# Kernel tuning notes

Hardware: AMD Instinct MI355X
Metric: run time of the kernel (lower is better)

The kernel has to match this reference:

```python
import jax, jax.numpy as jnp
import numpy as np

BATCH = 8192
IN_FEATURES = 1024
OUT_FEATURES = 1024
GRID_SIZE = 5
SPLINE_ORDER = 3
GRID_MIN, GRID_MAX = -1.0, 1.0
NUM_BASES = GRID_SIZE + SPLINE_ORDER  # 8
GRID_LEN = GRID_SIZE + 2 * SPLINE_ORDER + 1  # 12


def setup_inputs() -> dict:
    key = jax.random.key(0)
    k1, k2, k3 = jax.random.split(key, 3)
    x = jax.random.normal(k1, (BATCH, IN_FEATURES), dtype=jnp.float32)
    base_weight = jax.random.normal(k2, (OUT_FEATURES, IN_FEATURES), dtype=jnp.float32) * 0.1
    spline_weight = jax.random.normal(k3, (OUT_FEATURES, IN_FEATURES, NUM_BASES), dtype=jnp.float32) * 0.1
    grid = jnp.linspace(GRID_MIN, GRID_MAX, GRID_LEN, dtype=jnp.float32)  # buffer, not learned
    return {"x": x, "base_weight": base_weight, "spline_weight": spline_weight, "grid": grid}


def _bspline_basis(xc, grid, order):
    """Iterative Cox-de Boor DP, vectorized over all features and basis indices.
    xc: [B, F] clamped inputs; grid: [G] uniform knots (all denominators > 0).
    Returns [B, F, G - order - 1] = [B, F, NUM_BASES]."""
    G = grid.shape[0]
    xe = xc[..., None]  # [B, F, 1]
    # k = 0: indicator of knot interval, matches (x >= grid[i]) & (x < grid[i+1])
    B = ((xe >= grid[:-1]) & (xe < grid[1:])).astype(xc.dtype)  # [B, F, G-1]
    for k in range(1, order + 1):
        left = (xe - grid[: G - k - 1]) / (grid[k : G - 1] - grid[: G - k - 1]) * B[..., :-1]
        right = (grid[k + 1 : G] - xe) / (grid[k + 1 : G] - grid[1 : G - k]) * B[..., 1:]
        B = left + right  # [B, F, G-1-k]
    return B


def reference(x, base_weight, spline_weight, grid):
    # base path: SiLU activation then linear
    base_output = jax.nn.silu(x) @ base_weight.T  # [B, out]
    # spline path: B-spline basis per feature, weighted sum over (in, basis)
    x_clamped = jnp.clip(x, GRID_MIN * 0.99, GRID_MAX * 0.99)
    basis = _bspline_basis(x_clamped, grid, SPLINE_ORDER)  # [B, in, NUM_BASES]
    spline_output = jnp.einsum("bin,oin->bo", basis, spline_weight)
    return base_output + spline_output
```

## Files before the change

kernel.cpp:

```cpp
#include <hip/hip_runtime.h>
#include <stdint.h>

typedef _Float16 f16;
typedef __attribute__((ext_vector_type(8))) _Float16 f16x8;
typedef __attribute__((ext_vector_type(4))) float f32x4;

#define BATCH 8192
#define INF   1024
#define OUTF  1024
#define KTOT  9216
#define NT    72
#define CONV_BLOCKS 4608

__device__ __forceinline__ void gload16(const void* g, void* l) {
  __builtin_amdgcn_global_load_lds(
      (const __attribute__((address_space(1))) uint32_t*)g,
      (__attribute__((address_space(3))) uint32_t*)l, 16, 0, 0);
}

__global__ __launch_bounds__(256) void fused_prep_kernel(
    const float* __restrict__ bw, const float* __restrict__ sw,
    const float* __restrict__ x, const float* __restrict__ grid,
    f16* __restrict__ Wb, f16* __restrict__ Abuf)
{
  int blk = blockIdx.x;
  if (blk < CONV_BLOCKS) {
    int idx = blk * 256 + threadIdx.x;
    int o = idx / 1152;
    int r = idx - o * 1152;
    int k8 = r * 8;
    const float* src = (k8 < INF) ? (bw + (size_t)o * INF + k8)
                                  : (sw + (size_t)o * (INF * 8) + (k8 - INF));
    float4 v0 = *(const float4*)src;
    float4 v1 = *(const float4*)(src + 4);
    f16x8 ov;
    ov[0] = (f16)v0.x; ov[1] = (f16)v0.y; ov[2] = (f16)v0.z; ov[3] = (f16)v0.w;
    ov[4] = (f16)v1.x; ov[5] = (f16)v1.y; ov[6] = (f16)v1.z; ov[7] = (f16)v1.w;
    *(f16x8*)(Wb + (size_t)o * KTOT + k8) = ov;
    return;
  }

  int q = (blk - CONV_BLOCKS) * 256 + threadIdx.x;
  int b = q >> 8;
  int i0 = (q & 255) << 2;
  float4 xv = *(const float4*)(x + ((size_t)b << 10) + i0);
  float xa[4] = {xv.x, xv.y, xv.z, xv.w};

  float g[12];
#pragma unroll
  for (int j = 0; j < 12; ++j) g[j] = grid[j];
  float H  = g[1] - g[0];
  float r1 = 1.0f / H;
  float r2 = 0.5f * r1;
  float r3 = (1.0f / 3.0f) * r1;

  f16 sil[4];
  f16x8 bas[4];
#pragma unroll
  for (int e = 0; e < 4; ++e) {
    float v = xa[e];
    sil[e] = (f16)(v / (1.0f + __expf(-v)));
    float xe = fminf(fmaxf(v, -0.99f), 0.99f);
    float Bv[11];
#pragma unroll
    for (int j = 0; j < 11; ++j) Bv[j] = (xe >= g[j] && xe < g[j + 1]) ? 1.0f : 0.0f;
#pragma unroll
    for (int j = 0; j < 10; ++j) Bv[j] = (xe - g[j]) * r1 * Bv[j] + (g[j + 2] - xe) * r1 * Bv[j + 1];
#pragma unroll
    for (int j = 0; j < 9; ++j)  Bv[j] = (xe - g[j]) * r2 * Bv[j] + (g[j + 3] - xe) * r2 * Bv[j + 1];
#pragma unroll
    for (int j = 0; j < 8; ++j)  Bv[j] = (xe - g[j]) * r3 * Bv[j] + (g[j + 4] - xe) * r3 * Bv[j + 1];
#pragma unroll
    for (int n = 0; n < 8; ++n) bas[e][n] = (f16)Bv[n];
  }
  f16* row = Abuf + (size_t)b * KTOT;
  *(uint64_t*)(row + i0) = *(const uint64_t*)sil;
  f16* bp = row + INF + (size_t)i0 * 8;
#pragma unroll
  for (int e = 0; e < 4; ++e) *(f16x8*)(bp + e * 8) = bas[e];
}

#define LDA(base, m, s) (*(const f16x8*)((base) + (((m)*16 + la) * 64 + ((((s)*4 + lb) ^ lasw) * 8))))
#define LDB(base, n, s) (*(const f16x8*)((base) + ((wcn*64 + (n)*16 + la) * 64 + ((((s)*4 + lb) ^ lasw) * 8))))

#define MFMA1(m, n, s) acc[m][n] = __builtin_amdgcn_mfma_f32_16x16x32_f16(af[m][s], bf[n][s], acc[m][n], 0, 0, 0)
#define MFMA_S0(m0) do { \
  MFMA1(m0,0,0);   MFMA1(m0,1,0);   MFMA1(m0,2,0);   MFMA1(m0,3,0); \
  MFMA1(m0+1,0,0); MFMA1(m0+1,1,0); MFMA1(m0+1,2,0); MFMA1(m0+1,3,0); } while (0)
#define MFMA_S1(m0) do { \
  MFMA1(m0,0,1);   MFMA1(m0,1,1);   MFMA1(m0,2,1);   MFMA1(m0,3,1); \
  MFMA1(m0+1,0,1); MFMA1(m0+1,1,1); MFMA1(m0+1,2,1); MFMA1(m0+1,3,1); } while (0)

#define SCHED0 __builtin_amdgcn_sched_barrier(0)
#define SBARF  do { SCHED0; __builtin_amdgcn_s_barrier(); SCHED0; } while (0)
#define LGKM0  do { asm volatile("s_waitcnt lgkmcnt(0)" ::: "memory"); SCHED0; } while (0)

template <bool ATOMIC>
__global__ __launch_bounds__(256, 2) void kan_gemm_kernel(
    const f16* __restrict__ A, const f16* __restrict__ W,
    float* __restrict__ C, float* __restrict__ P1)
{
  __shared__ __align__(16) f16 lsA[128 * 64];
  __shared__ __align__(16) f16 lsB[256 * 64];

  const size_t K = KTOT;
  int bid = blockIdx.x;
  int xcd = bid & 7;
  int u   = bid >> 3;
  int tm  = xcd * 8 + (u & 7);
  int tn  = (u >> 3) & 3;
  int split = u >> 5;
  size_t kbase = (size_t)split * (NT * 64);

  int tid = threadIdx.x;
  int w = tid >> 6, l = tid & 63;
  int wcn = w;
  int la = l & 15, lb = l >> 4, lasw = la & 7;

  int rh = tid >> 3;
  int sc = (tid & 7) ^ (rh & 7);
  const f16* aSrc0 = A + (size_t)(tm * 128 + rh) * K + kbase + sc * 8;
  const f16* bSrc0 = W + (size_t)(tn * 256 + rh) * K + kbase + sc * 8;

  auto stageA = [&](int t) {
    size_t koff = (size_t)t * 64;
#pragma unroll
    for (int ln = 0; ln < 4; ++ln)
      gload16(aSrc0 + (size_t)ln * 32 * K + koff, lsA + ln * 2048 + w * 512);
  };
  auto stageB = [&](int t) {
    size_t koff = (size_t)t * 64;
#pragma unroll
    for (int ln = 0; ln < 8; ++ln)
      gload16(bSrc0 + (size_t)ln * 32 * K + koff, lsB + ln * 2048 + w * 512);
  };

  f16x8 af[8][2], bf[4][2];
  f32x4 acc[8][4] = {};

  stageA(0); stageB(0);

  for (int t = 0; t < NT; ++t) {
    asm volatile("s_waitcnt vmcnt(0)" ::: "memory");
    SBARF;

    bf[0][0] = LDB(lsB, 0, 0); bf[1][0] = LDB(lsB, 1, 0);
    bf[2][0] = LDB(lsB, 2, 0); bf[3][0] = LDB(lsB, 3, 0);
    bf[0][1] = LDB(lsB, 0, 1); bf[1][1] = LDB(lsB, 1, 1);
    bf[2][1] = LDB(lsB, 2, 1); bf[3][1] = LDB(lsB, 3, 1);
    af[0][0] = LDA(lsA, 0, 0); af[0][1] = LDA(lsA, 0, 1);
    af[1][0] = LDA(lsA, 1, 0); af[1][1] = LDA(lsA, 1, 1);
    __builtin_amdgcn_s_setprio(1);
    af[2][0] = LDA(lsA, 2, 0); af[3][0] = LDA(lsA, 3, 0);
    MFMA_S0(0);
    af[2][1] = LDA(lsA, 2, 1); af[3][1] = LDA(lsA, 3, 1);
    MFMA_S1(0);
    af[4][0] = LDA(lsA, 4, 0); af[5][0] = LDA(lsA, 5, 0);
    af[4][1] = LDA(lsA, 4, 1); af[5][1] = LDA(lsA, 5, 1);
    MFMA_S0(2);
    af[6][0] = LDA(lsA, 6, 0); af[7][0] = LDA(lsA, 7, 0);
    af[6][1] = LDA(lsA, 6, 1); af[7][1] = LDA(lsA, 7, 1);
    MFMA_S1(2);
    __builtin_amdgcn_s_setprio(0);

    LGKM0;
    SBARF;

    if (t < NT - 1) { stageA(t + 1); stageB(t + 1); }
    __builtin_amdgcn_s_setprio(1);
    MFMA_S0(4); MFMA_S1(4);
    MFMA_S0(6); MFMA_S1(6);
    __builtin_amdgcn_s_setprio(0);
  }

  int rowBase = tm * 128 + lb * 4;
  int colBase = tn * 256 + wcn * 64 + la;
  float* dst = ATOMIC ? C : (split ? P1 : C);
#pragma unroll
  for (int m = 0; m < 8; ++m)
#pragma unroll
    for (int n = 0; n < 4; ++n) {
      int col = colBase + n * 16;
#pragma unroll
      for (int j = 0; j < 4; ++j) {
        int row = rowBase + m * 16 + j;
        if (ATOMIC) atomicAdd(&C[(size_t)row * OUTF + col], acc[m][n][j]);
        else        dst[(size_t)row * OUTF + col] = acc[m][n][j];
      }
    }
}

__global__ __launch_bounds__(256) void reduce_kernel(
    float* __restrict__ out, const float* __restrict__ p)
{
  size_t i = ((size_t)blockIdx.x * 256 + threadIdx.x) * 4;
  f32x4 a = *(f32x4*)(out + i);
  f32x4 b = *(const f32x4*)(p + i);
  a += b;
  *(f32x4*)(out + i) = a;
}

extern "C" void kernel_launch(void* const* d_in, const int* in_sizes, int n_in,
                              void* d_out, int out_size, void* d_ws, size_t ws_size,
                              hipStream_t stream)
{
  const float* x  = (const float*)d_in[0];
  const float* bw = (const float*)d_in[1];
  const float* sw = (const float*)d_in[2];
  const float* gr = (const float*)d_in[3];
  float* out = (float*)d_out;

  f16* Wb = (f16*)d_ws;
  size_t wBytes = (size_t)OUTF * KTOT * sizeof(f16);
  f16* Abuf = (f16*)((char*)d_ws + wBytes);
  size_t aBytes = (size_t)BATCH * KTOT * sizeof(f16);
  size_t oBytes = (size_t)BATCH * OUTF * sizeof(float);

  int prepBlocks = (BATCH * INF / 4) / 256;
  fused_prep_kernel<<<CONV_BLOCKS + prepBlocks, 256, 0, stream>>>(
      bw, sw, x, gr, Wb, Abuf);

  if (ws_size >= wBytes + aBytes + oBytes) {
    float* P1 = (float*)((char*)d_ws + wBytes + aBytes);
    kan_gemm_kernel<false><<<512, 256, 0, stream>>>(Abuf, Wb, out, P1);
    reduce_kernel<<<(int)(oBytes / sizeof(float) / 4 / 256), 256, 0, stream>>>(out, P1);
  } else {
    hipMemsetAsync(d_out, 0, oBytes, stream);
    kan_gemm_kernel<true><<<512, 256, 0, stream>>>(Abuf, Wb, out, nullptr);
  }
}
```

Before: 205.6 us.

## Pre-swizzle weights into MFMA fragment layout and load B directly to registers

```diff
diff --git a/kernel.cpp b/kernel.cpp
--- a/kernel.cpp
+++ b/kernel.cpp
@@ -10,6 +10,7 @@
 #define OUTF  1024
 #define KTOT  9216
 #define NT    72
+#define NKT   144
 #define CONV_BLOCKS 4608
 
 __device__ __forceinline__ void gload16(const void* g, void* l) {
@@ -21,7 +22,7 @@
 __global__ __launch_bounds__(256) void fused_prep_kernel(
     const float* __restrict__ bw, const float* __restrict__ sw,
     const float* __restrict__ x, const float* __restrict__ grid,
-    f16* __restrict__ Wb, f16* __restrict__ Abuf)
+    f16* __restrict__ Wc, f16* __restrict__ Abuf)
 {
   int blk = blockIdx.x;
   if (blk < CONV_BLOCKS) {
@@ -36,7 +37,12 @@
     f16x8 ov;
     ov[0] = (f16)v0.x; ov[1] = (f16)v0.y; ov[2] = (f16)v0.z; ov[3] = (f16)v0.w;
     ov[4] = (f16)v1.x; ov[5] = (f16)v1.y; ov[6] = (f16)v1.z; ov[7] = (f16)v1.w;
-    *(f16x8*)(Wb + (size_t)o * KTOT + k8) = ov;
+    int tn = o >> 8, rp = o & 255;
+    int wcn = rp >> 6, n = (rp >> 4) & 3, la = rp & 15;
+    int kt = r >> 3, c = r & 7, s = c >> 2, lb = c & 3;
+    size_t off = (size_t)(tn * NKT + kt) * 16384 + wcn * 4096
+               + (s * 4 + n) * 512 + (lb * 16 + la) * 8;
+    *(f16x8*)(Wc + off) = ov;
     return;
   }
 
@@ -81,27 +87,58 @@
 }
 
 #define LDA(base, m, s) (*(const f16x8*)((base) + (((m)*16 + la) * 64 + ((((s)*4 + lb) ^ lasw) * 8))))
-#define LDB(base, n, s) (*(const f16x8*)((base) + ((wcn*64 + (n)*16 + la) * 64 + ((((s)*4 + lb) ^ lasw) * 8))))
-
-#define MFMA1(m, n, s) acc[m][n] = __builtin_amdgcn_mfma_f32_16x16x32_f16(af[m][s], bf[n][s], acc[m][n], 0, 0, 0)
-#define MFMA_S0(m0) do { \
-  MFMA1(m0,0,0);   MFMA1(m0,1,0);   MFMA1(m0,2,0);   MFMA1(m0,3,0); \
-  MFMA1(m0+1,0,0); MFMA1(m0+1,1,0); MFMA1(m0+1,2,0); MFMA1(m0+1,3,0); } while (0)
-#define MFMA_S1(m0) do { \
-  MFMA1(m0,0,1);   MFMA1(m0,1,1);   MFMA1(m0,2,1);   MFMA1(m0,3,1); \
-  MFMA1(m0+1,0,1); MFMA1(m0+1,1,1); MFMA1(m0+1,2,1); MFMA1(m0+1,3,1); } while (0)
+
+#define MFMA1(m, n, s, BF) acc[m][n] = __builtin_amdgcn_mfma_f32_16x16x32_f16(af[m][s], BF[(s)*4+(n)], acc[m][n], 0, 0, 0)
+#define MFMA_S0(m0, BF) do { \
+  MFMA1(m0,0,0,BF);   MFMA1(m0,1,0,BF);   MFMA1(m0,2,0,BF);   MFMA1(m0,3,0,BF); \
+  MFMA1(m0+1,0,0,BF); MFMA1(m0+1,1,0,BF); MFMA1(m0+1,2,0,BF); MFMA1(m0+1,3,0,BF); } while (0)
+#define MFMA_S1(m0, BF) do { \
+  MFMA1(m0,0,1,BF);   MFMA1(m0,1,1,BF);   MFMA1(m0,2,1,BF);   MFMA1(m0,3,1,BF); \
+  MFMA1(m0+1,0,1,BF); MFMA1(m0+1,1,1,BF); MFMA1(m0+1,2,1,BF); MFMA1(m0+1,3,1,BF); } while (0)
 
 #define SCHED0 __builtin_amdgcn_sched_barrier(0)
 #define SBARF  do { SCHED0; __builtin_amdgcn_s_barrier(); SCHED0; } while (0)
 #define LGKM0  do { asm volatile("s_waitcnt lgkmcnt(0)" ::: "memory"); SCHED0; } while (0)
 
+#define TILE_BODY(bfC, bfN, t) do { \
+  asm volatile("s_waitcnt vmcnt(0)" ::: "memory"); \
+  SBARF; \
+  if ((t) < NT - 1) { \
+    const f16* bp_ = bSrc + (size_t)(ktbase + (t) + 1) * 16384; \
+    bfN[0] = *(const f16x8*)(bp_);          bfN[1] = *(const f16x8*)(bp_ + 512); \
+    bfN[2] = *(const f16x8*)(bp_ + 1024);   bfN[3] = *(const f16x8*)(bp_ + 1536); \
+    bfN[4] = *(const f16x8*)(bp_ + 2048);   bfN[5] = *(const f16x8*)(bp_ + 2560); \
+    bfN[6] = *(const f16x8*)(bp_ + 3072);   bfN[7] = *(const f16x8*)(bp_ + 3584); \
+  } \
+  af[0][0] = LDA(lsA, 0, 0); af[0][1] = LDA(lsA, 0, 1); \
+  af[1][0] = LDA(lsA, 1, 0); af[1][1] = LDA(lsA, 1, 1); \
+  __builtin_amdgcn_s_setprio(1); \
+  af[2][0] = LDA(lsA, 2, 0); af[3][0] = LDA(lsA, 3, 0); \
+  MFMA_S0(0, bfC); \
+  af[2][1] = LDA(lsA, 2, 1); af[3][1] = LDA(lsA, 3, 1); \
+  MFMA_S1(0, bfC); \
+  af[4][0] = LDA(lsA, 4, 0); af[5][0] = LDA(lsA, 5, 0); \
+  af[4][1] = LDA(lsA, 4, 1); af[5][1] = LDA(lsA, 5, 1); \
+  MFMA_S0(2, bfC); \
+  af[6][0] = LDA(lsA, 6, 0); af[7][0] = LDA(lsA, 7, 0); \
+  af[6][1] = LDA(lsA, 6, 1); af[7][1] = LDA(lsA, 7, 1); \
+  MFMA_S1(2, bfC); \
+  __builtin_amdgcn_s_setprio(0); \
+  LGKM0; \
+  SBARF; \
+  if ((t) < NT - 1) stageA((t) + 1); \
+  __builtin_amdgcn_s_setprio(1); \
+  MFMA_S0(4, bfC); MFMA_S1(4, bfC); \
+  MFMA_S0(6, bfC); MFMA_S1(6, bfC); \
+  __builtin_amdgcn_s_setprio(0); \
+} while (0)
+
 template <bool ATOMIC>
 __global__ __launch_bounds__(256, 2) void kan_gemm_kernel(
-    const f16* __restrict__ A, const f16* __restrict__ W,
+    const f16* __restrict__ A, const f16* __restrict__ Wc,
     float* __restrict__ C, float* __restrict__ P1)
 {
   __shared__ __align__(16) f16 lsA[128 * 64];
-  __shared__ __align__(16) f16 lsB[256 * 64];
 
   const size_t K = KTOT;
   int bid = blockIdx.x;
@@ -110,17 +147,16 @@
   int tm  = xcd * 8 + (u & 7);
   int tn  = (u >> 3) & 3;
   int split = u >> 5;
-  size_t kbase = (size_t)split * (NT * 64);
+  int ktbase = split * NT;
+  size_t kbase = (size_t)ktbase * 64;
 
   int tid = threadIdx.x;
   int w = tid >> 6, l = tid & 63;
-  int wcn = w;
   int la = l & 15, lb = l >> 4, lasw = la & 7;
 
   int rh = tid >> 3;
   int sc = (tid & 7) ^ (rh & 7);
   const f16* aSrc0 = A + (size_t)(tm * 128 + rh) * K + kbase + sc * 8;
-  const f16* bSrc0 = W + (size_t)(tn * 256 + rh) * K + kbase + sc * 8;
 
   auto stageA = [&](int t) {
     size_t koff = (size_t)t * 64;
@@ -128,53 +164,26 @@
     for (int ln = 0; ln < 4; ++ln)
       gload16(aSrc0 + (size_t)ln * 32 * K + koff, lsA + ln * 2048 + w * 512);
   };
-  auto stageB = [&](int t) {
-    size_t koff = (size_t)t * 64;
-#pragma unroll
-    for (int ln = 0; ln < 8; ++ln)
-      gload16(bSrc0 + (size_t)ln * 32 * K + koff, lsB + ln * 2048 + w * 512);
-  };
-
-  f16x8 af[8][2], bf[4][2];
+
+  const f16* bSrc = Wc + (size_t)tn * NKT * 16384 + w * 4096 + l * 8;
+
+  f16x8 af[8][2], bfX[8], bfY[8];
   f32x4 acc[8][4] = {};
 
-  stageA(0); stageB(0);
-
-  for (int t = 0; t < NT; ++t) {
-    asm volatile("s_waitcnt vmcnt(0)" ::: "memory");
-    SBARF;
-
-    bf[0][0] = LDB(lsB, 0, 0); bf[1][0] = LDB(lsB, 1, 0);
-    bf[2][0] = LDB(lsB, 2, 0); bf[3][0] = LDB(lsB, 3, 0);
-    bf[0][1] = LDB(lsB, 0, 1); bf[1][1] = LDB(lsB, 1, 1);
-    bf[2][1] = LDB(lsB, 2, 1); bf[3][1] = LDB(lsB, 3, 1);
-    af[0][0] = LDA(lsA, 0, 0); af[0][1] = LDA(lsA, 0, 1);
-    af[1][0] = LDA(lsA, 1, 0); af[1][1] = LDA(lsA, 1, 1);
-    __builtin_amdgcn_s_setprio(1);
-    af[2][0] = LDA(lsA, 2, 0); af[3][0] = LDA(lsA, 3, 0);
-    MFMA_S0(0);
-    af[2][1] = LDA(lsA, 2, 1); af[3][1] = LDA(lsA, 3, 1);
-    MFMA_S1(0);
-    af[4][0] = LDA(lsA, 4, 0); af[5][0] = LDA(lsA, 5, 0);
-    af[4][1] = LDA(lsA, 4, 1); af[5][1] = LDA(lsA, 5, 1);
-    MFMA_S0(2);
-    af[6][0] = LDA(lsA, 6, 0); af[7][0] = LDA(lsA, 7, 0);
-    af[6][1] = LDA(lsA, 6, 1); af[7][1] = LDA(lsA, 7, 1);
-    MFMA_S1(2);
-    __builtin_amdgcn_s_setprio(0);
-
-    LGKM0;
-    SBARF;
-
-    if (t < NT - 1) { stageA(t + 1); stageB(t + 1); }
-    __builtin_amdgcn_s_setprio(1);
-    MFMA_S0(4); MFMA_S1(4);
-    MFMA_S0(6); MFMA_S1(6);
-    __builtin_amdgcn_s_setprio(0);
+  {
+    const f16* bp_ = bSrc + (size_t)ktbase * 16384;
+#pragma unroll
+    for (int f = 0; f < 8; ++f) bfX[f] = *(const f16x8*)(bp_ + f * 512);
+  }
+  stageA(0);
+
+  for (int t = 0; t < NT; t += 2) {
+    TILE_BODY(bfX, bfY, t);
+    TILE_BODY(bfY, bfX, t + 1);
   }
 
   int rowBase = tm * 128 + lb * 4;
-  int colBase = tn * 256 + wcn * 64 + la;
+  int colBase = tn * 256 + w * 64 + la;
   float* dst = ATOMIC ? C : (split ? P1 : C);
 #pragma unroll
   for (int m = 0; m < 8; ++m)
@@ -210,7 +219,7 @@
   const float* gr = (const float*)d_in[3];
   float* out = (float*)d_out;
 
-  f16* Wb = (f16*)d_ws;
+  f16* Wc = (f16*)d_ws;
   size_t wBytes = (size_t)OUTF * KTOT * sizeof(f16);
   f16* Abuf = (f16*)((char*)d_ws + wBytes);
   size_t aBytes = (size_t)BATCH * KTOT * sizeof(f16);
@@ -218,14 +227,14 @@
 
   int prepBlocks = (BATCH * INF / 4) / 256;
   fused_prep_kernel<<<CONV_BLOCKS + prepBlocks, 256, 0, stream>>>(
-      bw, sw, x, gr, Wb, Abuf);
+      bw, sw, x, gr, Wc, Abuf);
 
   if (ws_size >= wBytes + aBytes + oBytes) {
     float* P1 = (float*)((char*)d_ws + wBytes + aBytes);
-    kan_gemm_kernel<false><<<512, 256, 0, stream>>>(Abuf, Wb, out, P1);
+    kan_gemm_kernel<false><<<512, 256, 0, stream>>>(Abuf, Wc, out, P1);
     reduce_kernel<<<(int)(oBytes / sizeof(float) / 4 / 256), 256, 0, stream>>>(out, P1);
   } else {
     hipMemsetAsync(d_out, 0, oBytes, stream);
-    kan_gemm_kernel<true><<<512, 256, 0, stream>>>(Abuf, Wb, out, nullptr);
-  }
-}
+    kan_gemm_kernel<true><<<512, 256, 0, stream>>>(Abuf, Wc, out, nullptr);
+  }
+}
```

Measured after the change: 220.7 us. +7.3%, slower.
